# Kernel tuning notes

Hardware: AMD Instinct MI355X
Metric: run time of the kernel (lower is better)

Reference implementation:

```python
import jax, jax.numpy as jnp
import numpy as np

STATE_LEN, SEQ_LEN, HIDDEN = 2048, 4096, 2048

def setup_inputs() -> dict:
    key = jax.random.key(0)
    k1, k2, k3, k4 = jax.random.split(key, 4)
    scale = 1.0 / np.sqrt(HIDDEN)
    return {
        "out_state": jax.random.normal(k1, (STATE_LEN, HIDDEN), dtype=jnp.float32),
        "history": jax.random.normal(k2, (SEQ_LEN, HIDDEN), dtype=jnp.float32),
        "W": jax.random.normal(k3, (HIDDEN, HIDDEN), dtype=jnp.float32) * scale,
        "b": jax.random.normal(k4, (HIDDEN,), dtype=jnp.float32) * scale,
    }

def reference(out_state, history, W, b):
    # method='general': energy_j = Linear(history_j) = history_j @ W.T + b
    # score[i, j] = out_state_i . energy_j  -> batched GEMM replacing the double loop
    energies = history @ W.T + b                 # [seq_len, hidden]
    scores = jnp.einsum('ih,jh->ij', out_state, energies)  # [state_len, seq_len]
    # F.softmax on a 2D tensor (legacy default) normalizes over dim=1 (rows)
    return jax.nn.softmax(scores, axis=-1)
```

## Files before the change

### kernel.cpp

```cpp
#include <hip/hip_runtime.h>


#define STATE_LEN 2048
#define SEQ_LEN   4096
#define HIDDEN    2048

#define BK 32

#define WAIT_VM8   0x0F78
#define WAIT_VM0   0x0F70
#define WAIT_LGKM0 0xC07F

typedef __bf16 bf16x8 __attribute__((ext_vector_type(8)));
typedef float f32x4 __attribute__((ext_vector_type(4)));

__device__ __forceinline__ unsigned short f32_to_bf16(float f) {
  unsigned u = __float_as_uint(f);
  u += 0x7FFFu + ((u >> 16) & 1u);
  return (unsigned short)(u >> 16);
}
__device__ __forceinline__ float bf16_to_f32(unsigned short h) {
  return __uint_as_float(((unsigned)h) << 16);
}

__device__ __forceinline__ void gld16(const void* g, void* l) {
  __builtin_amdgcn_global_load_lds(
      (const __attribute__((address_space(1))) unsigned int*)g,
      (__attribute__((address_space(3))) unsigned int*)l,
      16, 0, 0);
}

__global__ __launch_bounds__(256) void pack_all(
    const float* __restrict__ os, const float* __restrict__ hist,
    const float* __restrict__ W,
    unsigned short* __restrict__ ohi, unsigned short* __restrict__ olo,
    unsigned short* __restrict__ hhi, unsigned short* __restrict__ hlo,
    unsigned short* __restrict__ wthi, unsigned short* __restrict__ wtlo) {
  const int bx = blockIdx.x;
  const int t = threadIdx.x;
  if (bx >= 1024) {
    const int b2 = bx - 1024;
    const float* in;
    unsigned short *hi, *lo;
    int i;
    if (b2 < 2048) {
      in = os; hi = ohi; lo = olo; i = (b2 * 256 + t) * 8;
    } else {
      in = hist; hi = hhi; lo = hlo; i = ((b2 - 2048) * 256 + t) * 8;
    }
#pragma unroll
    for (int half = 0; half < 2; ++half) {
      float4 v = *(const float4*)&in[i + half * 4];
      ushort4 h, l;
      h.x = f32_to_bf16(v.x); l.x = f32_to_bf16(v.x - bf16_to_f32(h.x));
      h.y = f32_to_bf16(v.y); l.y = f32_to_bf16(v.y - bf16_to_f32(h.y));
      h.z = f32_to_bf16(v.z); l.z = f32_to_bf16(v.z - bf16_to_f32(h.z));
      h.w = f32_to_bf16(v.w); l.w = f32_to_bf16(v.w - bf16_to_f32(h.w));
      *(ushort4*)&hi[i + half * 4] = h;
      *(ushort4*)&lo[i + half * 4] = l;
    }
  } else {
    __shared__ float tile[64][65];
    const int bt = bx;
    const int h0 = (bt & 31) * 64;
    const int k0 = (bt >> 5) * 64;
    const int lr = t >> 4;
    const int c4 = (t & 15) * 4;
#pragma unroll
    for (int pass = 0; pass < 4; ++pass) {
      const int row = pass * 16 + lr;
      float4 v = *(const float4*)&W[(size_t)(h0 + row) * HIDDEN + k0 + c4];
      tile[row][c4] = v.x; tile[row][c4 + 1] = v.y;
      tile[row][c4 + 2] = v.z; tile[row][c4 + 3] = v.w;
    }
    __syncthreads();
#pragma unroll
    for (int pass = 0; pass < 4; ++pass) {
      const int kl = pass * 16 + (t >> 4);
      const int hl = (t & 15) * 4;
      ushort4 h4, l4;
#pragma unroll
      for (int j = 0; j < 4; ++j) {
        const float x = tile[hl + j][kl];
        const unsigned short h = f32_to_bf16(x);
        ((unsigned short*)&h4)[j] = h;
        ((unsigned short*)&l4)[j] = f32_to_bf16(x - bf16_to_f32(h));
      }
      const size_t o = (size_t)(k0 + kl) * HIDDEN + h0 + hl;
      *(ushort4*)&wthi[o] = h4;
      *(ushort4*)&wtlo[o] = l4;
    }
  }
}

__global__ __launch_bounds__(256) void reduce_split4(
    const float* __restrict__ p0, const float* __restrict__ p1,
    const float* __restrict__ p2, const float* __restrict__ p3,
    unsigned short* __restrict__ hi, unsigned short* __restrict__ lo, int n) {
  int i = (blockIdx.x * 256 + threadIdx.x) * 4;
  if (i >= n) return;
  float4 a = *(const float4*)&p0[i];
  float4 b = *(const float4*)&p1[i];
  float4 c = *(const float4*)&p2[i];
  float4 d = *(const float4*)&p3[i];
  a.x = (a.x + b.x) + (c.x + d.x);
  a.y = (a.y + b.y) + (c.y + d.y);
  a.z = (a.z + b.z) + (c.z + d.z);
  a.w = (a.w + b.w) + (c.w + d.w);
  ushort4 h, l;
  h.x = f32_to_bf16(a.x); l.x = f32_to_bf16(a.x - bf16_to_f32(h.x));
  h.y = f32_to_bf16(a.y); l.y = f32_to_bf16(a.y - bf16_to_f32(h.y));
  h.z = f32_to_bf16(a.z); l.z = f32_to_bf16(a.z - bf16_to_f32(h.z));
  h.w = f32_to_bf16(a.w); l.w = f32_to_bf16(a.w - bf16_to_f32(h.w));
  *(ushort4*)&hi[i] = h;
  *(ushort4*)&lo[i] = l;
}

template <int KSPLIT>
__global__ __launch_bounds__(512, 2) void gemm_big(
    const unsigned short* __restrict__ Ahi, const unsigned short* __restrict__ Alo,
    const unsigned short* __restrict__ Bhi, const unsigned short* __restrict__ Blo,
    float* __restrict__ P0, float* __restrict__ P1,
    float* __restrict__ P2, float* __restrict__ P3,
    int M, int N, int K) {
  __shared__ __align__(16) unsigned short sA[2][2][256 * BK];
  __shared__ __align__(16) unsigned short sB[2][2][256 * BK];

  const int t = threadIdx.x;

  const int gx = gridDim.x, gy = gridDim.y;
  int flat = blockIdx.x + gx * (blockIdx.y + gy * blockIdx.z);
  const int cpx = (gx * gy * gridDim.z) >> 3;
  flat = (flat & 7) * cpx + (flat >> 3);
  const int nbx = flat % gx;
  const int tq  = flat / gx;
  const int nby = tq % gy;
  const int nbz = tq / gy;

  const int tileM = nby * 256;
  const int tileN = nbx * 256;
  const int z = (KSPLIT > 1) ? nbz : 0;
  const int kBase = z * (K / KSPLIT);
  const int iters = (K / KSPLIT) / BK;
  float* Cf = (z == 0) ? P0 : (z == 1) ? P1 : (z == 2) ? P2 : P3;

  const int rr = t >> 2;
  const int cc = t & 3;

  const int lane = t & 63;
  const int wave = t >> 6;
  const int wm = wave >> 1;
  const int wn = wave & 1;
  const int lr = lane & 15;
  const int kqc = lane >> 4;

  f32x4 acc[4][8] = {};

  auto stage = [&](int buf, int k0) {
#pragma unroll
    for (int p = 0; p < 2; ++p) {
      const int r = p * 128 + rr;
      const int q = cc ^ ((r >> 1) & 3);
      const size_t ga = (size_t)(tileM + r) * K + k0 + q * 8;
      const size_t gb = (size_t)(tileN + r) * K + k0 + q * 8;
      const int ls = r * BK + cc * 8;
      gld16(Ahi + ga, &sA[buf][0][ls]);
      gld16(Alo + ga, &sA[buf][1][ls]);
      gld16(Bhi + gb, &sB[buf][0][ls]);
      gld16(Blo + gb, &sB[buf][1][ls]);
    }
  };

  stage(0, kBase);

  for (int it = 0; it < iters; ++it) {
    const int buf = it & 1;

    if (it + 1 < iters) {
      stage(buf ^ 1, kBase + (it + 1) * BK);
      __builtin_amdgcn_s_waitcnt(WAIT_VM8);
    } else {
      __builtin_amdgcn_s_waitcnt(WAIT_VM0);
    }
    __builtin_amdgcn_s_barrier();

    bf16x8 ah[4], al[4];
#pragma unroll
    for (int mi = 0; mi < 4; ++mi) {
      const int R = wm * 64 + mi * 16 + lr;
      const int off = R * BK + (kqc ^ ((R >> 1) & 3)) * 8;
      ah[mi] = *(const bf16x8*)&sA[buf][0][off];
      al[mi] = *(const bf16x8*)&sA[buf][1][off];
    }
#pragma unroll
    for (int nh = 0; nh < 2; ++nh) {
      bf16x8 bh[4], bl[4];
#pragma unroll
      for (int nj = 0; nj < 4; ++nj) {
        const int R = wn * 128 + (nh * 4 + nj) * 16 + lr;
        const int off = R * BK + (kqc ^ ((R >> 1) & 3)) * 8;
        bh[nj] = *(const bf16x8*)&sB[buf][0][off];
        bl[nj] = *(const bf16x8*)&sB[buf][1][off];
      }
#pragma unroll
      for (int mi = 0; mi < 4; ++mi)
#pragma unroll
        for (int nj = 0; nj < 4; ++nj) {
          f32x4 a = acc[mi][nh * 4 + nj];
          a = __builtin_amdgcn_mfma_f32_16x16x32_bf16(ah[mi], bh[nj], a, 0, 0, 0);
          a = __builtin_amdgcn_mfma_f32_16x16x32_bf16(ah[mi], bl[nj], a, 0, 0, 0);
          a = __builtin_amdgcn_mfma_f32_16x16x32_bf16(al[mi], bh[nj], a, 0, 0, 0);
          acc[mi][nh * 4 + nj] = a;
        }
    }

    __builtin_amdgcn_s_waitcnt(WAIT_LGKM0);
    __builtin_amdgcn_s_barrier();
  }

#pragma unroll
  for (int mi = 0; mi < 4; ++mi)
#pragma unroll
    for (int ni = 0; ni < 8; ++ni)
#pragma unroll
      for (int e = 0; e < 4; ++e) {
        const int row = tileM + wm * 64 + mi * 16 + (lane >> 4) * 4 + e;
        const int col = tileN + wn * 128 + ni * 16 + lr;
        Cf[(size_t)row * N + col] = acc[mi][ni][e];
      }
}

__global__ __launch_bounds__(256) void softmax_rows2(
    float* __restrict__ d, const float* __restrict__ p1, int cols) {
  const int row = blockIdx.x;
  float* p = d + (size_t)row * cols;
  const float* q = p1 + (size_t)row * cols;
  const int t = threadIdx.x;
  const int lane = t & 63;
  const int wave = t >> 6;
  __shared__ float sred[4];

  float4 v[4];
  float m = -3.0e38f;
#pragma unroll
  for (int k = 0; k < 4; ++k) {
    float4 a = *(const float4*)&p[(t + k * 256) * 4];
    float4 b = *(const float4*)&q[(t + k * 256) * 4];
    a.x += b.x; a.y += b.y; a.z += b.z; a.w += b.w;
    v[k] = a;
    m = fmaxf(m, fmaxf(fmaxf(a.x, a.y), fmaxf(a.z, a.w)));
  }
#pragma unroll
  for (int off = 32; off > 0; off >>= 1) m = fmaxf(m, __shfl_xor(m, off, 64));
  if (lane == 0) sred[wave] = m;
  __syncthreads();
  m = fmaxf(fmaxf(sred[0], sred[1]), fmaxf(sred[2], sred[3]));
  __syncthreads();

  float s = 0.f;
#pragma unroll
  for (int k = 0; k < 4; ++k) {
    v[k].x = __expf(v[k].x - m);
    v[k].y = __expf(v[k].y - m);
    v[k].z = __expf(v[k].z - m);
    v[k].w = __expf(v[k].w - m);
    s += (v[k].x + v[k].y) + (v[k].z + v[k].w);
  }
#pragma unroll
  for (int off = 32; off > 0; off >>= 1) s += __shfl_xor(s, off, 64);
  if (lane == 0) sred[wave] = s;
  __syncthreads();
  s = (sred[0] + sred[1]) + (sred[2] + sred[3]);
  const float inv = 1.0f / s;
#pragma unroll
  for (int k = 0; k < 4; ++k) {
    v[k].x *= inv; v[k].y *= inv; v[k].z *= inv; v[k].w *= inv;
    *(float4*)&p[(t + k * 256) * 4] = v[k];
  }
}

extern "C" void kernel_launch(void* const* d_in, const int* in_sizes, int n_in,
                              void* d_out, int out_size, void* d_ws, size_t ws_size,
                              hipStream_t stream) {
  const float* out_state = (const float*)d_in[0];
  const float* history   = (const float*)d_in[1];
  const float* W         = (const float*)d_in[2];
  float* out = (float*)d_out;

  char* ws = (char*)d_ws;
  const size_t MB = 1ull << 20;
  unsigned short* ohi  = (unsigned short*)(ws + 0 * MB);
  unsigned short* olo  = (unsigned short*)(ws + 8 * MB);
  unsigned short* wthi = (unsigned short*)(ws + 16 * MB);
  unsigned short* wtlo = (unsigned short*)(ws + 24 * MB);
  unsigned short* hhi  = (unsigned short*)(ws + 32 * MB);
  unsigned short* hlo  = (unsigned short*)(ws + 48 * MB);
  float*          pws  = (float*)(ws + 64 * MB);

  const size_t QSZ = (size_t)STATE_LEN * HIDDEN;
  float* g1p0 = pws;
  float* g1p1 = pws + QSZ;
  float* g1p2 = out;
  float* g1p3 = out + QSZ;
  unsigned short* thi = (unsigned short*)(ws + 0 * MB);
  unsigned short* tlo = (unsigned short*)(ws + 8 * MB);

  pack_all<<<7168, 256, 0, stream>>>(out_state, history, W, ohi, olo, hhi, hlo,
                                     wthi, wtlo);
  gemm_big<4><<<dim3(HIDDEN / 256, STATE_LEN / 256, 4), 512, 0, stream>>>(
      ohi, olo, wthi, wtlo, g1p0, g1p1, g1p2, g1p3, STATE_LEN, HIDDEN, HIDDEN);
  reduce_split4<<<(STATE_LEN * HIDDEN) / 1024, 256, 0, stream>>>(
      g1p0, g1p1, g1p2, g1p3, thi, tlo, STATE_LEN * HIDDEN);
  gemm_big<2><<<dim3(SEQ_LEN / 256, STATE_LEN / 256, 2), 512, 0, stream>>>(
      thi, tlo, hhi, hlo, out, pws, nullptr, nullptr, STATE_LEN, SEQ_LEN, HIDDEN);
  softmax_rows2<<<STATE_LEN, 256, 0, stream>>>(out, pws, SEQ_LEN);
}
```

Baseline: 272.3 us.

## Fuse pack, both GEMMs, reduction and softmax into one cooperative kernel

Replaces the five separate launches (pack, split-K GEMM, reduce, second GEMM, softmax) with one persistent cooperative kernel of 256 blocks, one per CU. The stages are separated by grid.sync plus thread fences, and the GEMM body is shared as a device function. The goal is to remove the launch gaps and tail bubbles between kernels. In exchange there are four grid-wide barriers, and the memory-bound pack, reduce and softmax phases now run with fewer threads in grid-stride loops, which may lower their achieved bandwidth.

```diff
diff --git a/kernel.cpp b/kernel.cpp
--- a/kernel.cpp
+++ b/kernel.cpp
@@ -1,4 +1,7 @@
 #include <hip/hip_runtime.h>
+#include <hip/hip_cooperative_groups.h>
+
+namespace cg = cooperative_groups;
 
 
 #define STATE_LEN 2048
@@ -30,120 +33,29 @@
       16, 0, 0);
 }
 
-__global__ __launch_bounds__(256) void pack_all(
-    const float* __restrict__ os, const float* __restrict__ hist,
-    const float* __restrict__ W,
-    unsigned short* __restrict__ ohi, unsigned short* __restrict__ olo,
-    unsigned short* __restrict__ hhi, unsigned short* __restrict__ hlo,
-    unsigned short* __restrict__ wthi, unsigned short* __restrict__ wtlo) {
-  const int bx = blockIdx.x;
-  const int t = threadIdx.x;
-  if (bx >= 1024) {
-    const int b2 = bx - 1024;
-    const float* in;
-    unsigned short *hi, *lo;
-    int i;
-    if (b2 < 2048) {
-      in = os; hi = ohi; lo = olo; i = (b2 * 256 + t) * 8;
-    } else {
-      in = hist; hi = hhi; lo = hlo; i = ((b2 - 2048) * 256 + t) * 8;
-    }
-#pragma unroll
-    for (int half = 0; half < 2; ++half) {
-      float4 v = *(const float4*)&in[i + half * 4];
-      ushort4 h, l;
-      h.x = f32_to_bf16(v.x); l.x = f32_to_bf16(v.x - bf16_to_f32(h.x));
-      h.y = f32_to_bf16(v.y); l.y = f32_to_bf16(v.y - bf16_to_f32(h.y));
-      h.z = f32_to_bf16(v.z); l.z = f32_to_bf16(v.z - bf16_to_f32(h.z));
-      h.w = f32_to_bf16(v.w); l.w = f32_to_bf16(v.w - bf16_to_f32(h.w));
-      *(ushort4*)&hi[i + half * 4] = h;
-      *(ushort4*)&lo[i + half * 4] = l;
-    }
-  } else {
-    __shared__ float tile[64][65];
-    const int bt = bx;
-    const int h0 = (bt & 31) * 64;
-    const int k0 = (bt >> 5) * 64;
-    const int lr = t >> 4;
-    const int c4 = (t & 15) * 4;
-#pragma unroll
-    for (int pass = 0; pass < 4; ++pass) {
-      const int row = pass * 16 + lr;
-      float4 v = *(const float4*)&W[(size_t)(h0 + row) * HIDDEN + k0 + c4];
-      tile[row][c4] = v.x; tile[row][c4 + 1] = v.y;
-      tile[row][c4 + 2] = v.z; tile[row][c4 + 3] = v.w;
-    }
-    __syncthreads();
-#pragma unroll
-    for (int pass = 0; pass < 4; ++pass) {
-      const int kl = pass * 16 + (t >> 4);
-      const int hl = (t & 15) * 4;
-      ushort4 h4, l4;
-#pragma unroll
-      for (int j = 0; j < 4; ++j) {
-        const float x = tile[hl + j][kl];
-        const unsigned short h = f32_to_bf16(x);
-        ((unsigned short*)&h4)[j] = h;
-        ((unsigned short*)&l4)[j] = f32_to_bf16(x - bf16_to_f32(h));
-      }
-      const size_t o = (size_t)(k0 + kl) * HIDDEN + h0 + hl;
-      *(ushort4*)&wthi[o] = h4;
-      *(ushort4*)&wtlo[o] = l4;
-    }
-  }
-}
-
-__global__ __launch_bounds__(256) void reduce_split4(
-    const float* __restrict__ p0, const float* __restrict__ p1,
-    const float* __restrict__ p2, const float* __restrict__ p3,
-    unsigned short* __restrict__ hi, unsigned short* __restrict__ lo, int n) {
-  int i = (blockIdx.x * 256 + threadIdx.x) * 4;
-  if (i >= n) return;
-  float4 a = *(const float4*)&p0[i];
-  float4 b = *(const float4*)&p1[i];
-  float4 c = *(const float4*)&p2[i];
-  float4 d = *(const float4*)&p3[i];
-  a.x = (a.x + b.x) + (c.x + d.x);
-  a.y = (a.y + b.y) + (c.y + d.y);
-  a.z = (a.z + b.z) + (c.z + d.z);
-  a.w = (a.w + b.w) + (c.w + d.w);
-  ushort4 h, l;
-  h.x = f32_to_bf16(a.x); l.x = f32_to_bf16(a.x - bf16_to_f32(h.x));
-  h.y = f32_to_bf16(a.y); l.y = f32_to_bf16(a.y - bf16_to_f32(h.y));
-  h.z = f32_to_bf16(a.z); l.z = f32_to_bf16(a.z - bf16_to_f32(h.z));
-  h.w = f32_to_bf16(a.w); l.w = f32_to_bf16(a.w - bf16_to_f32(h.w));
-  *(ushort4*)&hi[i] = h;
-  *(ushort4*)&lo[i] = l;
-}
-
-template <int KSPLIT>
-__global__ __launch_bounds__(512, 2) void gemm_big(
+__device__ __forceinline__ void split8(const float* __restrict__ in,
+                                       unsigned short* __restrict__ hi,
+                                       unsigned short* __restrict__ lo, int i) {
+#pragma unroll
+  for (int half = 0; half < 2; ++half) {
+    float4 v = *(const float4*)&in[i + half * 4];
+    ushort4 h, l;
+    h.x = f32_to_bf16(v.x); l.x = f32_to_bf16(v.x - bf16_to_f32(h.x));
+    h.y = f32_to_bf16(v.y); l.y = f32_to_bf16(v.y - bf16_to_f32(h.y));
+    h.z = f32_to_bf16(v.z); l.z = f32_to_bf16(v.z - bf16_to_f32(h.z));
+    h.w = f32_to_bf16(v.w); l.w = f32_to_bf16(v.w - bf16_to_f32(h.w));
+    *(ushort4*)&hi[i + half * 4] = h;
+    *(ushort4*)&lo[i + half * 4] = l;
+  }
+}
+
+__device__ __forceinline__ void gemm_stage(
     const unsigned short* __restrict__ Ahi, const unsigned short* __restrict__ Alo,
     const unsigned short* __restrict__ Bhi, const unsigned short* __restrict__ Blo,
-    float* __restrict__ P0, float* __restrict__ P1,
-    float* __restrict__ P2, float* __restrict__ P3,
-    int M, int N, int K) {
-  __shared__ __align__(16) unsigned short sA[2][2][256 * BK];
-  __shared__ __align__(16) unsigned short sB[2][2][256 * BK];
-
+    float* __restrict__ Cf, int tileM, int tileN, int kBase, int iters,
+    int N, int K,
+    unsigned short (*sA)[2][256 * BK], unsigned short (*sB)[2][256 * BK]) {
   const int t = threadIdx.x;
-
-  const int gx = gridDim.x, gy = gridDim.y;
-  int flat = blockIdx.x + gx * (blockIdx.y + gy * blockIdx.z);
-  const int cpx = (gx * gy * gridDim.z) >> 3;
-  flat = (flat & 7) * cpx + (flat >> 3);
-  const int nbx = flat % gx;
-  const int tq  = flat / gx;
-  const int nby = tq % gy;
-  const int nbz = tq / gy;
-
-  const int tileM = nby * 256;
-  const int tileN = nbx * 256;
-  const int z = (KSPLIT > 1) ? nbz : 0;
-  const int kBase = z * (K / KSPLIT);
-  const int iters = (K / KSPLIT) / BK;
-  float* Cf = (z == 0) ? P0 : (z == 1) ? P1 : (z == 2) ? P2 : P3;
-
   const int rr = t >> 2;
   const int cc = t & 3;
 
@@ -230,52 +142,170 @@
       }
 }
 
-__global__ __launch_bounds__(256) void softmax_rows2(
-    float* __restrict__ d, const float* __restrict__ p1, int cols) {
-  const int row = blockIdx.x;
-  float* p = d + (size_t)row * cols;
-  const float* q = p1 + (size_t)row * cols;
+__global__ __launch_bounds__(512, 2) void fused_all(
+    const float* __restrict__ os, const float* __restrict__ hist,
+    const float* __restrict__ W,
+    unsigned short* __restrict__ ohi, unsigned short* __restrict__ olo,
+    unsigned short* __restrict__ hhi, unsigned short* __restrict__ hlo,
+    unsigned short* __restrict__ wthi, unsigned short* __restrict__ wtlo,
+    float* __restrict__ g1p0, float* __restrict__ g1p1,
+    float* __restrict__ g1p2, float* __restrict__ g1p3,
+    unsigned short* __restrict__ thi, unsigned short* __restrict__ tlo,
+    float* __restrict__ out, float* __restrict__ p1out) {
+  __shared__ __align__(16) unsigned short sA[2][2][256 * BK];
+  __shared__ __align__(16) unsigned short sB[2][2][256 * BK];
+
+  cg::grid_group grid = cg::this_grid();
   const int t = threadIdx.x;
-  const int lane = t & 63;
-  const int wave = t >> 6;
-  __shared__ float sred[4];
-
-  float4 v[4];
-  float m = -3.0e38f;
-#pragma unroll
-  for (int k = 0; k < 4; ++k) {
-    float4 a = *(const float4*)&p[(t + k * 256) * 4];
-    float4 b = *(const float4*)&q[(t + k * 256) * 4];
-    a.x += b.x; a.y += b.y; a.z += b.z; a.w += b.w;
-    v[k] = a;
-    m = fmaxf(m, fmaxf(fmaxf(a.x, a.y), fmaxf(a.z, a.w)));
-  }
-#pragma unroll
-  for (int off = 32; off > 0; off >>= 1) m = fmaxf(m, __shfl_xor(m, off, 64));
-  if (lane == 0) sred[wave] = m;
-  __syncthreads();
-  m = fmaxf(fmaxf(sred[0], sred[1]), fmaxf(sred[2], sred[3]));
-  __syncthreads();
-
-  float s = 0.f;
-#pragma unroll
-  for (int k = 0; k < 4; ++k) {
-    v[k].x = __expf(v[k].x - m);
-    v[k].y = __expf(v[k].y - m);
-    v[k].z = __expf(v[k].z - m);
-    v[k].w = __expf(v[k].w - m);
-    s += (v[k].x + v[k].y) + (v[k].z + v[k].w);
-  }
-#pragma unroll
-  for (int off = 32; off > 0; off >>= 1) s += __shfl_xor(s, off, 64);
-  if (lane == 0) sred[wave] = s;
-  __syncthreads();
-  s = (sred[0] + sred[1]) + (sred[2] + sred[3]);
-  const float inv = 1.0f / s;
-#pragma unroll
-  for (int k = 0; k < 4; ++k) {
-    v[k].x *= inv; v[k].y *= inv; v[k].z *= inv; v[k].w *= inv;
-    *(float4*)&p[(t + k * 256) * 4] = v[k];
+  const int b = blockIdx.x;
+  const int gtid = b * 512 + t;
+
+  {
+    const int h = t >> 8;
+    const int tt = t & 255;
+    float (*tile)[65] = (float(*)[65])((char*)sA + h * 32768);
+    const int lr = tt >> 4;
+    const int c4 = (tt & 15) * 4;
+#pragma unroll
+    for (int rep = 0; rep < 2; ++rep) {
+      const int bt = (b * 2 + h) * 2 + rep;
+      const int h0 = (bt & 31) * 64;
+      const int k0 = (bt >> 5) * 64;
+      __syncthreads();
+#pragma unroll
+      for (int pass = 0; pass < 4; ++pass) {
+        const int row = pass * 16 + lr;
+        float4 v = *(const float4*)&W[(size_t)(h0 + row) * HIDDEN + k0 + c4];
+        tile[row][c4] = v.x; tile[row][c4 + 1] = v.y;
+        tile[row][c4 + 2] = v.z; tile[row][c4 + 3] = v.w;
+      }
+      __syncthreads();
+#pragma unroll
+      for (int pass = 0; pass < 4; ++pass) {
+        const int kl = pass * 16 + (tt >> 4);
+        const int hl = (tt & 15) * 4;
+        ushort4 h4, l4;
+#pragma unroll
+        for (int j = 0; j < 4; ++j) {
+          const float x = tile[hl + j][kl];
+          const unsigned short hh = f32_to_bf16(x);
+          ((unsigned short*)&h4)[j] = hh;
+          ((unsigned short*)&l4)[j] = f32_to_bf16(x - bf16_to_f32(hh));
+        }
+        const size_t o = (size_t)(k0 + kl) * HIDDEN + h0 + hl;
+        *(ushort4*)&wthi[o] = h4;
+        *(ushort4*)&wtlo[o] = l4;
+      }
+    }
+    for (int u = gtid; u < (STATE_LEN * HIDDEN) / 8; u += 131072)
+      split8(os, ohi, olo, u * 8);
+    for (int u = gtid; u < (SEQ_LEN * HIDDEN) / 8; u += 131072)
+      split8(hist, hhi, hlo, u * 8);
+  }
+  __threadfence();
+  grid.sync();
+
+  {
+    int flat = (b & 7) * 32 + (b >> 3);
+    const int nbx = flat & 7;
+    const int nby = (flat >> 3) & 7;
+    const int nbz = flat >> 6;
+    float* Cf = (nbz == 0) ? g1p0 : (nbz == 1) ? g1p1 : (nbz == 2) ? g1p2 : g1p3;
+    gemm_stage(ohi, olo, wthi, wtlo, Cf, nby * 256, nbx * 256, nbz * 512, 16,
+               HIDDEN, HIDDEN, sA, sB);
+  }
+  __threadfence();
+  grid.sync();
+
+  {
+    const int n4 = (STATE_LEN * HIDDEN) / 4;
+    for (int u = gtid; u < n4; u += 131072) {
+      const int i = u * 4;
+      float4 a = *(const float4*)&g1p0[i];
+      float4 bb = *(const float4*)&g1p1[i];
+      float4 c = *(const float4*)&g1p2[i];
+      float4 d = *(const float4*)&g1p3[i];
+      a.x = (a.x + bb.x) + (c.x + d.x);
+      a.y = (a.y + bb.y) + (c.y + d.y);
+      a.z = (a.z + bb.z) + (c.z + d.z);
+      a.w = (a.w + bb.w) + (c.w + d.w);
+      ushort4 h, l;
+      h.x = f32_to_bf16(a.x); l.x = f32_to_bf16(a.x - bf16_to_f32(h.x));
+      h.y = f32_to_bf16(a.y); l.y = f32_to_bf16(a.y - bf16_to_f32(h.y));
+      h.z = f32_to_bf16(a.z); l.z = f32_to_bf16(a.z - bf16_to_f32(h.z));
+      h.w = f32_to_bf16(a.w); l.w = f32_to_bf16(a.w - bf16_to_f32(h.w));
+      *(ushort4*)&thi[i] = h;
+      *(ushort4*)&tlo[i] = l;
+    }
+  }
+  __threadfence();
+  grid.sync();
+
+  {
+    int flat = (b & 7) * 32 + (b >> 3);
+    const int nbx = flat & 15;
+    const int q = flat >> 4;
+    const int nby = q & 7;
+    const int nbz = q >> 3;
+    float* Cf = (nbz == 0) ? out : p1out;
+    gemm_stage(thi, tlo, hhi, hlo, Cf, nby * 256, nbx * 256, nbz * 1024, 32,
+               SEQ_LEN, HIDDEN, sA, sB);
+  }
+  __threadfence();
+  grid.sync();
+
+  {
+    float* sred = (float*)&sB[0][0][0];
+    const int lane = t & 63;
+    const int wave = t >> 6;
+    for (int rr = 0; rr < 8; ++rr) {
+      __syncthreads();
+      const int row = b * 8 + rr;
+      float* p = out + (size_t)row * SEQ_LEN;
+      const float* q = p1out + (size_t)row * SEQ_LEN;
+      const int base = t * 8;
+
+      float4 v[2];
+      float m = -3.0e38f;
+#pragma unroll
+      for (int k = 0; k < 2; ++k) {
+        float4 a = *(const float4*)&p[base + k * 4];
+        float4 bb = *(const float4*)&q[base + k * 4];
+        a.x += bb.x; a.y += bb.y; a.z += bb.z; a.w += bb.w;
+        v[k] = a;
+        m = fmaxf(m, fmaxf(fmaxf(a.x, a.y), fmaxf(a.z, a.w)));
+      }
+#pragma unroll
+      for (int off = 32; off > 0; off >>= 1) m = fmaxf(m, __shfl_xor(m, off, 64));
+      if (lane == 0) sred[wave] = m;
+      __syncthreads();
+      m = sred[0];
+#pragma unroll
+      for (int w = 1; w < 8; ++w) m = fmaxf(m, sred[w]);
+
+      float s = 0.f;
+#pragma unroll
+      for (int k = 0; k < 2; ++k) {
+        v[k].x = __expf(v[k].x - m);
+        v[k].y = __expf(v[k].y - m);
+        v[k].z = __expf(v[k].z - m);
+        v[k].w = __expf(v[k].w - m);
+        s += (v[k].x + v[k].y) + (v[k].z + v[k].w);
+      }
+#pragma unroll
+      for (int off = 32; off > 0; off >>= 1) s += __shfl_xor(s, off, 64);
+      __syncthreads();
+      if (lane == 0) sred[wave] = s;
+      __syncthreads();
+      s = ((sred[0] + sred[1]) + (sred[2] + sred[3])) +
+          ((sred[4] + sred[5]) + (sred[6] + sred[7]));
+      const float inv = 1.0f / s;
+#pragma unroll
+      for (int k = 0; k < 2; ++k) {
+        v[k].x *= inv; v[k].y *= inv; v[k].z *= inv; v[k].w *= inv;
+        *(float4*)&p[base + k * 4] = v[k];
+      }
+    }
   }
 }
 
@@ -304,14 +334,14 @@
   float* g1p3 = out + QSZ;
   unsigned short* thi = (unsigned short*)(ws + 0 * MB);
   unsigned short* tlo = (unsigned short*)(ws + 8 * MB);
-
-  pack_all<<<7168, 256, 0, stream>>>(out_state, history, W, ohi, olo, hhi, hlo,
-                                     wthi, wtlo);
-  gemm_big<4><<<dim3(HIDDEN / 256, STATE_LEN / 256, 4), 512, 0, stream>>>(
-      ohi, olo, wthi, wtlo, g1p0, g1p1, g1p2, g1p3, STATE_LEN, HIDDEN, HIDDEN);
-  reduce_split4<<<(STATE_LEN * HIDDEN) / 1024, 256, 0, stream>>>(
-      g1p0, g1p1, g1p2, g1p3, thi, tlo, STATE_LEN * HIDDEN);
-  gemm_big<2><<<dim3(SEQ_LEN / 256, STATE_LEN / 256, 2), 512, 0, stream>>>(
-      thi, tlo, hhi, hlo, out, pws, nullptr, nullptr, STATE_LEN, SEQ_LEN, HIDDEN);
-  softmax_rows2<<<STATE_LEN, 256, 0, stream>>>(out, pws, SEQ_LEN);
-}
+  float* p1out = pws;
+
+  void* args[] = {
+      (void*)&out_state, (void*)&history, (void*)&W,
+      (void*)&ohi, (void*)&olo, (void*)&hhi, (void*)&hlo,
+      (void*)&wthi, (void*)&wtlo,
+      (void*)&g1p0, (void*)&g1p1, (void*)&g1p2, (void*)&g1p3,
+      (void*)&thi, (void*)&tlo, (void*)&out, (void*)&p1out};
+  hipLaunchCooperativeKernel(reinterpret_cast<void*>(fused_all), dim3(256),
+                             dim3(512), args, 0, stream);
+}
```

Result: slower. 729.3 us (+167.8%).

## Replace split-K first GEMM and reduce with 128-tile GEMM emitting bf16 split

Applied to the files above, without the earlier changes.

The first GEMM (out_state x W) used to be split four ways along K, writing fp32 partials that a separate kernel summed and split into hi/lo bf16. It is now a single-pass 128x128-tile GEMM with 256 threads that converts its accumulators straight to hi/lo bf16. This removes the partial-buffer traffic and one kernel launch. In exchange each block runs the full K loop, the grid has 256 blocks instead of 256x4 partial tiles, and the epilogue writes scalar ushorts, which may lower parallelism and store efficiency.

```diff
diff --git a/kernel.cpp b/kernel.cpp
--- a/kernel.cpp
+++ b/kernel.cpp
@@ -93,27 +93,103 @@
   }
 }
 
-__global__ __launch_bounds__(256) void reduce_split4(
-    const float* __restrict__ p0, const float* __restrict__ p1,
-    const float* __restrict__ p2, const float* __restrict__ p3,
-    unsigned short* __restrict__ hi, unsigned short* __restrict__ lo, int n) {
-  int i = (blockIdx.x * 256 + threadIdx.x) * 4;
-  if (i >= n) return;
-  float4 a = *(const float4*)&p0[i];
-  float4 b = *(const float4*)&p1[i];
-  float4 c = *(const float4*)&p2[i];
-  float4 d = *(const float4*)&p3[i];
-  a.x = (a.x + b.x) + (c.x + d.x);
-  a.y = (a.y + b.y) + (c.y + d.y);
-  a.z = (a.z + b.z) + (c.z + d.z);
-  a.w = (a.w + b.w) + (c.w + d.w);
-  ushort4 h, l;
-  h.x = f32_to_bf16(a.x); l.x = f32_to_bf16(a.x - bf16_to_f32(h.x));
-  h.y = f32_to_bf16(a.y); l.y = f32_to_bf16(a.y - bf16_to_f32(h.y));
-  h.z = f32_to_bf16(a.z); l.z = f32_to_bf16(a.z - bf16_to_f32(h.z));
-  h.w = f32_to_bf16(a.w); l.w = f32_to_bf16(a.w - bf16_to_f32(h.w));
-  *(ushort4*)&hi[i] = h;
-  *(ushort4*)&lo[i] = l;
+__global__ __launch_bounds__(256, 2) void gemm_t128(
+    const unsigned short* __restrict__ Ahi, const unsigned short* __restrict__ Alo,
+    const unsigned short* __restrict__ Bhi, const unsigned short* __restrict__ Blo,
+    unsigned short* __restrict__ Thi, unsigned short* __restrict__ Tlo) {
+  __shared__ __align__(16) unsigned short sA[2][2][128 * BK];
+  __shared__ __align__(16) unsigned short sB[2][2][128 * BK];
+
+  const int t = threadIdx.x;
+
+  int flat = blockIdx.x + 16 * blockIdx.y;
+  flat = (flat & 7) * 32 + (flat >> 3);
+  const int tileN = (flat & 15) * 128;
+  const int tileM = (flat >> 4) * 128;
+  const int K = HIDDEN, N = HIDDEN;
+
+  const int rr = t >> 2;
+  const int cc = t & 3;
+
+  const int lane = t & 63;
+  const int wave = t >> 6;
+  const int wm = wave >> 1;
+  const int wn = wave & 1;
+  const int lr = lane & 15;
+  const int kqc = lane >> 4;
+
+  f32x4 acc[4][4] = {};
+
+  auto stage = [&](int buf, int k0) {
+#pragma unroll
+    for (int p = 0; p < 2; ++p) {
+      const int r = p * 64 + rr;
+      const int q = cc ^ ((r >> 1) & 3);
+      const size_t ga = (size_t)(tileM + r) * K + k0 + q * 8;
+      const size_t gb = (size_t)(tileN + r) * K + k0 + q * 8;
+      const int ls = r * BK + cc * 8;
+      gld16(Ahi + ga, &sA[buf][0][ls]);
+      gld16(Alo + ga, &sA[buf][1][ls]);
+      gld16(Bhi + gb, &sB[buf][0][ls]);
+      gld16(Blo + gb, &sB[buf][1][ls]);
+    }
+  };
+
+  stage(0, 0);
+
+  const int iters = K / BK;
+  for (int it = 0; it < iters; ++it) {
+    const int buf = it & 1;
+    if (it + 1 < iters) {
+      stage(buf ^ 1, (it + 1) * BK);
+      __builtin_amdgcn_s_waitcnt(WAIT_VM8);
+    } else {
+      __builtin_amdgcn_s_waitcnt(WAIT_VM0);
+    }
+    __builtin_amdgcn_s_barrier();
+
+    bf16x8 ah[4], al[4], bh[4], bl[4];
+#pragma unroll
+    for (int mi = 0; mi < 4; ++mi) {
+      const int R = wm * 64 + mi * 16 + lr;
+      const int off = R * BK + (kqc ^ ((R >> 1) & 3)) * 8;
+      ah[mi] = *(const bf16x8*)&sA[buf][0][off];
+      al[mi] = *(const bf16x8*)&sA[buf][1][off];
+    }
+#pragma unroll
+    for (int ni = 0; ni < 4; ++ni) {
+      const int R = wn * 64 + ni * 16 + lr;
+      const int off = R * BK + (kqc ^ ((R >> 1) & 3)) * 8;
+      bh[ni] = *(const bf16x8*)&sB[buf][0][off];
+      bl[ni] = *(const bf16x8*)&sB[buf][1][off];
+    }
+#pragma unroll
+    for (int mi = 0; mi < 4; ++mi)
+#pragma unroll
+      for (int ni = 0; ni < 4; ++ni) {
+        acc[mi][ni] = __builtin_amdgcn_mfma_f32_16x16x32_bf16(ah[mi], bh[ni], acc[mi][ni], 0, 0, 0);
+        acc[mi][ni] = __builtin_amdgcn_mfma_f32_16x16x32_bf16(ah[mi], bl[ni], acc[mi][ni], 0, 0, 0);
+        acc[mi][ni] = __builtin_amdgcn_mfma_f32_16x16x32_bf16(al[mi], bh[ni], acc[mi][ni], 0, 0, 0);
+      }
+
+    __builtin_amdgcn_s_waitcnt(WAIT_LGKM0);
+    __builtin_amdgcn_s_barrier();
+  }
+
+#pragma unroll
+  for (int mi = 0; mi < 4; ++mi)
+#pragma unroll
+    for (int ni = 0; ni < 4; ++ni)
+#pragma unroll
+      for (int e = 0; e < 4; ++e) {
+        const int row = tileM + wm * 64 + mi * 16 + (lane >> 4) * 4 + e;
+        const int col = tileN + wn * 64 + ni * 16 + lr;
+        const float v = acc[mi][ni][e];
+        const unsigned short h = f32_to_bf16(v);
+        const size_t o = (size_t)row * N + col;
+        Thi[o] = h;
+        Tlo[o] = f32_to_bf16(v - bf16_to_f32(h));
+      }
 }
 
 template <int KSPLIT>
@@ -121,7 +197,6 @@
     const unsigned short* __restrict__ Ahi, const unsigned short* __restrict__ Alo,
     const unsigned short* __restrict__ Bhi, const unsigned short* __restrict__ Blo,
     float* __restrict__ P0, float* __restrict__ P1,
-    float* __restrict__ P2, float* __restrict__ P3,
     int M, int N, int K) {
   __shared__ __align__(16) unsigned short sA[2][2][256 * BK];
   __shared__ __align__(16) unsigned short sB[2][2][256 * BK];
@@ -142,7 +217,7 @@
   const int z = (KSPLIT > 1) ? nbz : 0;
   const int kBase = z * (K / KSPLIT);
   const int iters = (K / KSPLIT) / BK;
-  float* Cf = (z == 0) ? P0 : (z == 1) ? P1 : (z == 2) ? P2 : P3;
+  float* Cf = (z == 0) ? P0 : P1;
 
   const int rr = t >> 2;
   const int cc = t & 3;
@@ -244,7 +319,7 @@
   float m = -3.0e38f;
 #pragma unroll
   for (int k = 0; k < 4; ++k) {
-    float4 a = *(const float4*)&p[(t + k * 256) * 4];
+    float4 a = *(float4*)&p[(t + k * 256) * 4];
     float4 b = *(const float4*)&q[(t + k * 256) * 4];
     a.x += b.x; a.y += b.y; a.z += b.z; a.w += b.w;
     v[k] = a;
@@ -295,23 +370,14 @@
   unsigned short* wtlo = (unsigned short*)(ws + 24 * MB);
   unsigned short* hhi  = (unsigned short*)(ws + 32 * MB);
   unsigned short* hlo  = (unsigned short*)(ws + 48 * MB);
-  float*          pws  = (float*)(ws + 64 * MB);
-
-  const size_t QSZ = (size_t)STATE_LEN * HIDDEN;
-  float* g1p0 = pws;
-  float* g1p1 = pws + QSZ;
-  float* g1p2 = out;
-  float* g1p3 = out + QSZ;
-  unsigned short* thi = (unsigned short*)(ws + 0 * MB);
-  unsigned short* tlo = (unsigned short*)(ws + 8 * MB);
+  unsigned short* thi  = (unsigned short*)(ws + 64 * MB);
+  unsigned short* tlo  = (unsigned short*)(ws + 72 * MB);
+  float* p1out = (float*)(ws + 0 * MB);
 
   pack_all<<<7168, 256, 0, stream>>>(out_state, history, W, ohi, olo, hhi, hlo,
                                      wthi, wtlo);
-  gemm_big<4><<<dim3(HIDDEN / 256, STATE_LEN / 256, 4), 512, 0, stream>>>(
-      ohi, olo, wthi, wtlo, g1p0, g1p1, g1p2, g1p3, STATE_LEN, HIDDEN, HIDDEN);
-  reduce_split4<<<(STATE_LEN * HIDDEN) / 1024, 256, 0, stream>>>(
-      g1p0, g1p1, g1p2, g1p3, thi, tlo, STATE_LEN * HIDDEN);
+  gemm_t128<<<dim3(16, 16), 256, 0, stream>>>(ohi, olo, wthi, wtlo, thi, tlo);
   gemm_big<2><<<dim3(SEQ_LEN / 256, STATE_LEN / 256, 2), 512, 0, stream>>>(
-      thi, tlo, hhi, hlo, out, pws, nullptr, nullptr, STATE_LEN, SEQ_LEN, HIDDEN);
-  softmax_rows2<<<STATE_LEN, 256, 0, stream>>>(out, pws, SEQ_LEN);
-}
+      thi, tlo, hhi, hlo, out, p1out, STATE_LEN, SEQ_LEN, HIDDEN);
+  softmax_rows2<<<STATE_LEN, 256, 0, stream>>>(out, p1out, SEQ_LEN);
+}
```

New measurement: 289.3 us. 6.2% more time.
